# Kernel tuning notes

Measured on AMD Instinct MI355X. Metric: run time of the kernel, lower is better.

The kernel has to match this reference:

```python
import jax, jax.numpy as jnp
import numpy as np

N = 50000       # nodes
E = 800000      # edges
D = 128         # in_channels == hidden*heads
H = 8           # heads
C = 16          # hidden_channels (per-head dim)
L = 4           # num_layers
OUT = 128       # out_channels


def setup_inputs() -> dict:
    key = jax.random.key(0)
    ks = jax.random.split(key, 16)
    s = 1.0 / np.sqrt(D)
    inp = {
        "x": jax.random.normal(ks[0], (N, D), dtype=jnp.float32),
        "edge_index": jax.random.randint(ks[1], (2, E), 0, N, dtype=jnp.int32),
        "batch": jnp.zeros((N,), dtype=jnp.int32),
        # stacked per-layer params (all layers are D->H*C with D == H*C)
        "Wq": jax.random.normal(ks[2], (L, D, H * C), dtype=jnp.float32) * s,
        "bq": jnp.zeros((L, H * C), dtype=jnp.float32),
        "Wk": jax.random.normal(ks[3], (L, D, H * C), dtype=jnp.float32) * s,
        "bk": jnp.zeros((L, H * C), dtype=jnp.float32),
        "Wv": jax.random.normal(ks[4], (L, D, H * C), dtype=jnp.float32) * s,
        "bv": jnp.zeros((L, H * C), dtype=jnp.float32),
        "Wskip": jax.random.normal(ks[5], (L, D, H * C), dtype=jnp.float32) * s,
        "bskip": jnp.zeros((L, H * C), dtype=jnp.float32),
        "Wout": jax.random.normal(ks[6], (D, OUT), dtype=jnp.float32) * s,
        "bout": jnp.zeros((OUT,), dtype=jnp.float32),
    }
    return inp


def _transformer_conv(x, src, dst, Wq, bq, Wk, bk, Wv, bv, Wskip, bskip):
    # PyG TransformerConv (concat=True, root_weight=True, beta=False), eval mode
    q = (x @ Wq + bq).reshape(N, H, C)
    k = (x @ Wk + bk).reshape(N, H, C)
    v = (x @ Wv + bv).reshape(N, H, C)
    # edge-wise attention scores [E, H]
    score = jnp.einsum("ehc,ehc->eh", q[dst], k[src]) / jnp.sqrt(jnp.float32(C))
    # segment softmax over incoming edges of each dst node
    m = jax.ops.segment_max(score, dst, num_segments=N)          # [N, H]
    p = jnp.exp(score - m[dst])                                  # [E, H]
    z = jax.ops.segment_sum(p, dst, num_segments=N)              # [N, H]
    alpha = p / z[dst]                                           # [E, H]
    msg = alpha[:, :, None] * v[src]                             # [E, H, C]
    agg = jax.ops.segment_sum(msg, dst, num_segments=N)          # [N, H, C]
    return agg.reshape(N, H * C) + (x @ Wskip + bskip)


def reference(x, edge_index, batch, Wq, bq, Wk, bk, Wv, bv, Wskip, bskip, Wout, bout):
    src = edge_index[0]
    dst = edge_index[1]
    for l in range(L):
        x = _transformer_conv(x, src, dst, Wq[l], bq[l], Wk[l], bk[l],
                              Wv[l], bv[l], Wskip[l], bskip[l])
        x = jax.nn.relu(x)  # dropout is identity in eval mode
    return x @ Wout + bout
```

## Files before the change

kernel.cpp:

```cpp
#include <hip/hip_runtime.h>
#include <hip/hip_fp16.h>
#include <math.h>

#define NN 50000
#define EE 800000
#define DD 128

typedef __attribute__((ext_vector_type(8))) _Float16 half8;
typedef __attribute__((ext_vector_type(2))) _Float16 h2;
typedef __attribute__((ext_vector_type(4))) float f32x4;

#if __has_builtin(__builtin_amdgcn_fdot2)
#define FDOT2(a,b,c) __builtin_amdgcn_fdot2((a),(b),(c),false)
#else
static __device__ __forceinline__ float FDOT2(h2 a, h2 b, float c){
  return c + (float)a[0]*(float)b[0] + (float)a[1]*(float)b[1];
}
#endif


__global__ void zero_kernel(int* __restrict__ p, int n){
  int i = blockIdx.x*blockDim.x + threadIdx.x;
  if (i < n) p[i] = 0;
}

__global__ void hist_kernel(const int* __restrict__ edst, int* __restrict__ deg, int e){
  int i = blockIdx.x*blockDim.x + threadIdx.x;
  if (i < e) atomicAdd(&deg[edst[i]], 1);
}

__global__ void scan_partial(const int* __restrict__ deg, int* __restrict__ bsum, int n){
  __shared__ int s[256];
  int t = threadIdx.x;
  int i = blockIdx.x*256 + t;
  s[t] = (i < n) ? deg[i] : 0;
  __syncthreads();
  for (int o = 128; o > 0; o >>= 1){
    if (t < o) s[t] += s[t+o];
    __syncthreads();
  }
  if (t == 0) bsum[blockIdx.x] = s[0];
}

__global__ void scan_bsums(int* __restrict__ bsum, int nb){
  __shared__ int s[256];
  int t = threadIdx.x;
  int v = (t < nb) ? bsum[t] : 0;
  s[t] = v;
  __syncthreads();
  for (int o = 1; o < 256; o <<= 1){
    int x = (t >= o) ? s[t-o] : 0;
    __syncthreads();
    s[t] += x;
    __syncthreads();
  }
  if (t < nb) bsum[t] = s[t] - v;
}

__global__ void scan_apply(const int* __restrict__ deg, const int* __restrict__ bsum,
                           int* __restrict__ off, int* __restrict__ cursor, int n){
  __shared__ int s[256];
  int t = threadIdx.x;
  int i = blockIdx.x*256 + t;
  int v = (i < n) ? deg[i] : 0;
  s[t] = v;
  __syncthreads();
  for (int o = 1; o < 256; o <<= 1){
    int x = (t >= o) ? s[t-o] : 0;
    __syncthreads();
    s[t] += x;
    __syncthreads();
  }
  int excl = s[t] - v + bsum[blockIdx.x];
  if (i < n){
    off[i] = excl;
    if (i < n-1) cursor[i] = excl;
  }
}

__global__ void scatter_kernel(const int* __restrict__ esrc, const int* __restrict__ edst,
                               int* __restrict__ cursor, int* __restrict__ csr_src, int e){
  int i = blockIdx.x*blockDim.x + threadIdx.x;
  if (i < e){
    int d = edst[i];
    int pos = atomicAdd(&cursor[d], 1);
    csr_src[pos] = esrc[i];
  }
}

__global__ void prep_w(const float* __restrict__ Wq, const float* __restrict__ Wk,
                       const float* __restrict__ Wv, const float* __restrict__ Ws,
                       const float* __restrict__ bq, const float* __restrict__ bk,
                       const float* __restrict__ bv, const float* __restrict__ bs,
                       const float* __restrict__ Wout,
                       __half* __restrict__ wt, float* __restrict__ bcat,
                       __half* __restrict__ wtout){
  int idx = blockIdx.x*256 + threadIdx.x;
  if (idx < 4*512*128){
    int l = idx >> 16;
    int rem = idx & 65535;
    int n = rem >> 7;
    int k = rem & 127;
    int mat = n >> 7;
    int nn = n & 127;
    const float* W = (mat==0)?Wq:(mat==1)?Wk:(mat==2)?Wv:Ws;
    wt[idx] = __float2half(W[l*16384 + k*128 + nn]);
  }
  if (idx < 128*128){
    int n = idx >> 7, k = idx & 127;
    wtout[idx] = __float2half(Wout[k*128 + n]);
  }
  if (idx < 4*512){
    int l = idx >> 9, n = idx & 511;
    int mat = n >> 7, nn = n & 127;
    const float* B = (mat==0)?bq:(mat==1)?bk:(mat==2)?bv:bs;
    bcat[idx] = B[l*128 + nn];
  }
}

__global__ void convert_x(const float* __restrict__ x, __half* __restrict__ xh, int n8){
  int i = blockIdx.x*256 + threadIdx.x;
  if (i < n8){
    float4 f0 = *(const float4*)&x[(size_t)i*8];
    float4 f1 = *(const float4*)&x[(size_t)i*8+4];
    __half2 h[4] = {__floats2half2_rn(f0.x,f0.y), __floats2half2_rn(f0.z,f0.w),
                    __floats2half2_rn(f1.x,f1.y), __floats2half2_rn(f1.z,f1.w)};
    *(int4*)&xh[(size_t)i*8] = *(const int4*)h;
  }
}

template<int FMODE>
__global__ __launch_bounds__(256) void mfma_gemm(
    const __half* __restrict__ xh, const __half* __restrict__ wt,
    const float* __restrict__ bias,
    __half* __restrict__ oq, __half* __restrict__ okv, __half* __restrict__ osk,
    float* __restrict__ ofp, int nrows)
{
  __shared__ __half a_lds[64*128];
  __shared__ __half b_lds[128*128];

  const int tid = threadIdx.x;
  const int m0 = blockIdx.x * 64;
  const int lane = tid & 63;
  const int w  = tid >> 6;
  const int wr = w >> 1, wc = w & 1;
  const int li = lane & 15, lg = lane >> 4;

  #pragma unroll
  for (int p = 0; p < 4; p++){
    int chunk = tid + p*256;
    int row = chunk >> 4;
    int cs  = chunk & 15;
    int gm = m0 + row;
    int4 va = make_int4(0,0,0,0);
    if (gm < nrows) va = *(const int4*)&xh[(size_t)gm*DD + cs*8];
    *(int4*)&a_lds[row*128 + (cs ^ (row & 7))*8] = va;
  }

  const int NMATS = (FMODE == 0) ? 4 : 1;
  for (int mat = 0; mat < NMATS; mat++){
    #pragma unroll
    for (int p = 0; p < 8; p++){
      int chunk = tid + p*256;
      int row = chunk >> 4;
      int cs  = chunk & 15;
      int4 vb = *(const int4*)&wt[(size_t)(mat*128 + row)*DD + cs*8];
      *(int4*)&b_lds[row*128 + (cs ^ (row & 7))*8] = vb;
    }
    __syncthreads();

    f32x4 acc[2][4];
    #pragma unroll
    for (int fn = 0; fn < 4; fn++){
      float b = bias[mat*128 + wc*64 + fn*16 + li];
      #pragma unroll
      for (int fm = 0; fm < 2; fm++)
        acc[fm][fn] = (f32x4){b, b, b, b};
    }

    #pragma unroll
    for (int kk = 0; kk < 4; kk++){
      half8 af[2], bf[4];
      #pragma unroll
      for (int fm = 0; fm < 2; fm++){
        int row = wr*32 + fm*16 + li;
        int chunk = kk*4 + lg;
        af[fm] = *(half8*)&a_lds[row*128 + (chunk ^ (row & 7))*8];
      }
      #pragma unroll
      for (int fn = 0; fn < 4; fn++){
        int row = wc*64 + fn*16 + li;
        int chunk = kk*4 + lg;
        bf[fn] = *(half8*)&b_lds[row*128 + (chunk ^ (row & 7))*8];
      }
      #pragma unroll
      for (int fm = 0; fm < 2; fm++)
        #pragma unroll
        for (int fn = 0; fn < 4; fn++)
          acc[fm][fn] = __builtin_amdgcn_mfma_f32_16x16x32_f16(af[fm], bf[fn], acc[fm][fn], 0, 0, 0);
    }
    __syncthreads();

    if (FMODE == 0){
      #pragma unroll
      for (int fm = 0; fm < 2; fm++)
        #pragma unroll
        for (int fn = 0; fn < 4; fn++)
          #pragma unroll
          for (int r = 0; r < 4; r++){
            int row = wr*32 + fm*16 + lg*4 + r;
            int col = wc*64 + fn*16 + li;
            int chunk = col >> 3, within = col & 7;
            b_lds[row*128 + (chunk ^ (row & 7))*8 + within] = __float2half(acc[fm][fn][r]);
          }
      __syncthreads();
      #pragma unroll
      for (int p = 0; p < 4; p++){
        int chunk = tid + p*256;
        int row = chunk >> 4, cs = chunk & 15;
        int gm = m0 + row;
        if (gm < nrows){
          int4 val = *(int4*)&b_lds[row*128 + (cs ^ (row & 7))*8];
          if (mat == 0)      *(int4*)&oq [(size_t)gm*128 + cs*8]       = val;
          else if (mat == 1) *(int4*)&okv[(size_t)gm*256 + cs*8]       = val;
          else if (mat == 2) *(int4*)&okv[(size_t)gm*256 + 128 + cs*8] = val;
          else               *(int4*)&osk[(size_t)gm*128 + cs*8]       = val;
        }
      }
      __syncthreads();
    } else {
      float* f_lds = (float*)b_lds;
      #pragma unroll
      for (int fm = 0; fm < 2; fm++)
        #pragma unroll
        for (int fn = 0; fn < 4; fn++)
          #pragma unroll
          for (int r = 0; r < 4; r++){
            int row = wr*32 + fm*16 + lg*4 + r;
            int col = wc*64 + fn*16 + li;
            int chunk = col >> 2, within = col & 3;
            f_lds[row*128 + (chunk ^ (row & 7))*4 + within] = acc[fm][fn][r];
          }
      __syncthreads();
      #pragma unroll
      for (int p = 0; p < 8; p++){
        int chunk = tid + p*256;
        int row = chunk >> 5, cs = chunk & 31;
        int gm = m0 + row;
        if (gm < nrows)
          *(int4*)&ofp[(size_t)gm*DD + cs*4] = *(int4*)&f_lds[row*128 + (cs ^ (row & 7))*4];
      }
    }
  }
}

__global__ __launch_bounds__(256) void agg_kernel(
    const __half* __restrict__ hq, const __half* __restrict__ hsk,
    const __half* __restrict__ kv,
    const int* __restrict__ off, const int* __restrict__ csr_src,
    __half* __restrict__ xout, int n)
{
  int wid = blockIdx.x*4 + (threadIdx.x >> 6);
  if (wid >= n) return;
  int lane = threadIdx.x & 63;
  int sub  = lane >> 3;
  int h    = lane & 7;
  int c    = h*16;

  int4 q0 = *(const int4*)&hq[(size_t)wid*DD + c];
  int4 q1 = *(const int4*)&hq[(size_t)wid*DD + c + 8];
  const h2* qh0 = (const h2*)&q0;
  const h2* qh1 = (const h2*)&q1;

  float z = 0.f;
  float acc[16];
  #pragma unroll
  for (int i = 0; i < 16; i++) acc[i] = 0.f;

  const int e1 = off[wid+1];
  int e = off[wid] + sub;
  int s2 = (e+8 < e1) ? csr_src[e+8] : -1;
  int4 k0r, k1r, v0r, v1r;
  if (e < e1){
    const __half* r = kv + (size_t)csr_src[e]*256 + c;
    k0r = *(const int4*)r;        k1r = *(const int4*)(r+8);
    v0r = *(const int4*)(r+128);  v1r = *(const int4*)(r+136);
  }
  while (e < e1){
    int4 k0n, k1n, v0n, v1n;
    if (s2 >= 0){
      const __half* r = kv + (size_t)s2*256 + c;
      k0n = *(const int4*)r;        k1n = *(const int4*)(r+8);
      v0n = *(const int4*)(r+128);  v1n = *(const int4*)(r+136);
    }
    int s3 = (e+16 < e1) ? csr_src[e+16] : -1;

    const h2* kh0 = (const h2*)&k0r;
    const h2* kh1 = (const h2*)&k1r;
    float p = 0.f;
    #pragma unroll
    for (int i = 0; i < 4; i++) p = FDOT2(kh0[i], qh0[i], p);
    #pragma unroll
    for (int i = 0; i < 4; i++) p = FDOT2(kh1[i], qh1[i], p);
    float wgt = __expf(p * 0.25f);

    const __half2* vh0 = (const __half2*)&v0r;
    const __half2* vh1 = (const __half2*)&v1r;
    #pragma unroll
    for (int i = 0; i < 4; i++){
      float2 f = __half22float2(vh0[i]);
      acc[2*i]   += wgt * f.x;
      acc[2*i+1] += wgt * f.y;
    }
    #pragma unroll
    for (int i = 0; i < 4; i++){
      float2 f = __half22float2(vh1[i]);
      acc[8+2*i]   += wgt * f.x;
      acc[8+2*i+1] += wgt * f.y;
    }
    z += wgt;

    k0r = k0n; k1r = k1n; v0r = v0n; v1r = v1n;
    s2 = s3; e += 8;
  }

  #pragma unroll
  for (int d = 8; d <= 32; d <<= 1){
    z += __shfl_xor(z, d);
    #pragma unroll
    for (int i = 0; i < 16; i++)
      acc[i] += __shfl_xor(acc[i], d);
  }

  if (sub == 0){
    float inv = (z > 0.f) ? 1.f/z : 0.f;
    int4 s0 = *(const int4*)&hsk[(size_t)wid*DD + c];
    int4 s1 = *(const int4*)&hsk[(size_t)wid*DD + c + 8];
    const __half2* sh0 = (const __half2*)&s0;
    const __half2* sh1 = (const __half2*)&s1;
    __half2 po[4];
    #pragma unroll
    for (int i = 0; i < 4; i++){
      float2 s = __half22float2(sh0[i]);
      po[i] = __floats2half2_rn(fmaxf(acc[2*i]*inv + s.x, 0.f),
                                fmaxf(acc[2*i+1]*inv + s.y, 0.f));
    }
    *(int4*)&xout[(size_t)wid*DD + c] = *(const int4*)po;
    #pragma unroll
    for (int i = 0; i < 4; i++){
      float2 s = __half22float2(sh1[i]);
      po[i] = __floats2half2_rn(fmaxf(acc[8+2*i]*inv + s.x, 0.f),
                                fmaxf(acc[8+2*i+1]*inv + s.y, 0.f));
    }
    *(int4*)&xout[(size_t)wid*DD + c + 8] = *(const int4*)po;
  }
}


extern "C" void kernel_launch(void* const* d_in, const int* in_sizes, int n_in,
                              void* d_out, int out_size, void* d_ws, size_t ws_size,
                              hipStream_t stream) {
  const float* x     = (const float*)d_in[0];
  const int*   edge  = (const int*)d_in[1];
  const int*   esrc  = edge;
  const int*   edst  = edge + EE;
  const float* Wq    = (const float*)d_in[3];
  const float* bq    = (const float*)d_in[4];
  const float* Wk    = (const float*)d_in[5];
  const float* bk    = (const float*)d_in[6];
  const float* Wv    = (const float*)d_in[7];
  const float* bv    = (const float*)d_in[8];
  const float* Wsk   = (const float*)d_in[9];
  const float* bsk   = (const float*)d_in[10];
  const float* Wout  = (const float*)d_in[11];
  const float* bout  = (const float*)d_in[12];
  float* out = (float*)d_out;

  uintptr_t base = (uintptr_t)d_ws;
  auto align = [](uintptr_t p){ return (p + 255) & ~(uintptr_t)255; };
  int* deg    = (int*)base;  base = align(base + (NN+1)*sizeof(int));
  int* off    = (int*)base;  base = align(base + (NN+1)*sizeof(int));
  int* cursor = (int*)base;  base = align(base + NN*sizeof(int));
  int* bsum   = (int*)base;  base = align(base + 256*sizeof(int));
  int* csr    = (int*)base;  base = align(base + (size_t)EE*sizeof(int));
  __half* xh   = (__half*)base; base = align(base + (size_t)NN*DD*sizeof(__half));
  __half* xbuf = (__half*)base; base = align(base + (size_t)NN*DD*sizeof(__half));
  __half* hq   = (__half*)base; base = align(base + (size_t)NN*DD*sizeof(__half));
  __half* hsk  = (__half*)base; base = align(base + (size_t)NN*DD*sizeof(__half));
  __half* kvb  = (__half*)base; base = align(base + (size_t)NN*256*sizeof(__half));
  __half* wt   = (__half*)base; base = align(base + (size_t)4*512*128*sizeof(__half));
  __half* wtout= (__half*)base; base = align(base + (size_t)128*128*sizeof(__half));
  float*  bcat = (float*)base;  base = align(base + (size_t)4*512*sizeof(float));

  const int NP = NN + 1;
  const int SCAN_BLKS = (NP + 255)/256;

  zero_kernel<<<SCAN_BLKS, 256, 0, stream>>>(deg, NP);
  hist_kernel<<<(EE+255)/256, 256, 0, stream>>>(edst, deg, EE);
  scan_partial<<<SCAN_BLKS, 256, 0, stream>>>(deg, bsum, NP);
  scan_bsums<<<1, 256, 0, stream>>>(bsum, SCAN_BLKS);
  scan_apply<<<SCAN_BLKS, 256, 0, stream>>>(deg, bsum, off, cursor, NP);
  scatter_kernel<<<(EE+255)/256, 256, 0, stream>>>(esrc, edst, cursor, csr, EE);

  prep_w<<<1024, 256, 0, stream>>>(Wq, Wk, Wv, Wsk, bq, bk, bv, bsk, Wout, wt, bcat, wtout);
  convert_x<<<(NN*DD/8 + 255)/256, 256, 0, stream>>>(x, xh, NN*DD/8);

  const int MT64 = (NN + 63)/64;
  const __half* xin = xh;
  for (int l = 0; l < 4; l++){
    mfma_gemm<0><<<MT64, 256, 0, stream>>>(
        xin, wt + (size_t)l*512*128, bcat + l*512,
        hq, kvb, hsk, nullptr, NN);
    agg_kernel<<<(NN+3)/4, 256, 0, stream>>>(hq, hsk, kvb, off, csr, xbuf, NN);
    xin = xbuf;
  }
  mfma_gemm<1><<<MT64, 256, 0, stream>>>(
      xin, wtout, bout, nullptr, nullptr, nullptr, out, NN);
}
```

Baseline: 437.3 us.

## Store K/V head-major and split aggregation per head across blocks

The GEMM epilogue now writes K and V in a head-major layout ([head][node][k16|v16]), so each head's key and value sit together in one contiguous 64-byte chunk per source node. The aggregation kernel launches one block per (head, 4-node group): each wavefront processes 16 edges at once with 4 lanes per edge, and blockIdx.x&7 spreads consecutive blocks across heads. The aim is a smaller per-head working set for the random gathers, which may improve L2 hit rates, plus more parallelism per node. In exchange, csr offsets and indices are read 8 times (once per head), the q loads are redundant, and the old software prefetch of the next edge's K/V is dropped.

```diff
diff --git a/kernel.cpp b/kernel.cpp
--- a/kernel.cpp
+++ b/kernel.cpp
@@ -221,10 +221,13 @@
         int gm = m0 + row;
         if (gm < nrows){
           int4 val = *(int4*)&b_lds[row*128 + (cs ^ (row & 7))*8];
-          if (mat == 0)      *(int4*)&oq [(size_t)gm*128 + cs*8]       = val;
-          else if (mat == 1) *(int4*)&okv[(size_t)gm*256 + cs*8]       = val;
-          else if (mat == 2) *(int4*)&okv[(size_t)gm*256 + 128 + cs*8] = val;
-          else               *(int4*)&osk[(size_t)gm*128 + cs*8]       = val;
+          if (mat == 0)      *(int4*)&oq [(size_t)gm*128 + cs*8] = val;
+          else if (mat == 3) *(int4*)&osk[(size_t)gm*128 + cs*8] = val;
+          else {
+            int h = cs >> 1, half = cs & 1;
+            size_t base = ((size_t)h*NN + gm)*32 + ((mat==2) ? 16 : 0);
+            *(int4*)&okv[base + half*8] = val;
+          }
         }
       }
       __syncthreads();
@@ -256,103 +259,72 @@
 
 __global__ __launch_bounds__(256) void agg_kernel(
     const __half* __restrict__ hq, const __half* __restrict__ hsk,
-    const __half* __restrict__ kv,
+    const __half* __restrict__ kvh,
     const int* __restrict__ off, const int* __restrict__ csr_src,
     __half* __restrict__ xout, int n)
 {
-  int wid = blockIdx.x*4 + (threadIdx.x >> 6);
-  if (wid >= n) return;
-  int lane = threadIdx.x & 63;
-  int sub  = lane >> 3;
-  int h    = lane & 7;
-  int c    = h*16;
-
-  int4 q0 = *(const int4*)&hq[(size_t)wid*DD + c];
-  int4 q1 = *(const int4*)&hq[(size_t)wid*DD + c + 8];
-  const h2* qh0 = (const h2*)&q0;
-  const h2* qh1 = (const h2*)&q1;
+  const int h  = blockIdx.x & 7;
+  const int nd = (blockIdx.x >> 3)*4 + (threadIdx.x >> 6);
+  if (nd >= n) return;
+  const int lane  = threadIdx.x & 63;
+  const int eslot = lane >> 2;
+  const int part  = lane & 3;
+
+  int4 qr = make_int4(0,0,0,0);
+  if (part < 2) qr = *(const int4*)&hq[(size_t)nd*DD + h*16 + part*8];
+  const h2* qq = (const h2*)&qr;
 
   float z = 0.f;
-  float acc[16];
+  float acc[8] = {0.f,0.f,0.f,0.f,0.f,0.f,0.f,0.f};
+
+  const int e0 = off[nd], e1 = off[nd+1];
+  const __half* kvbase = kvh + (size_t)h*NN*32;
+  for (int eb = e0; eb < e1; eb += 16){
+    int e = eb + eslot;
+    bool valid = e < e1;
+    int ee = valid ? e : (e1 - 1);
+    int s = csr_src[ee];
+    int4 d = *(const int4*)&kvbase[(size_t)s*32 + part*8];
+
+    const h2* kd = (const h2*)&d;
+    float p = 0.f;
+    #pragma unroll
+    for (int i = 0; i < 4; i++) p = FDOT2(kd[i], qq[i], p);
+    p += __shfl_xor(p, 1);
+    float wgt = valid ? __expf(p * 0.25f) : 0.f;
+    float wv  = __shfl_xor(wgt, 2);
+
+    const __half2* vd = (const __half2*)&d;
+    #pragma unroll
+    for (int i = 0; i < 4; i++){
+      float2 f = __half22float2(vd[i]);
+      acc[2*i]   += wv * f.x;
+      acc[2*i+1] += wv * f.y;
+    }
+    z += wv;
+  }
+
   #pragma unroll
-  for (int i = 0; i < 16; i++) acc[i] = 0.f;
-
-  const int e1 = off[wid+1];
-  int e = off[wid] + sub;
-  int s2 = (e+8 < e1) ? csr_src[e+8] : -1;
-  int4 k0r, k1r, v0r, v1r;
-  if (e < e1){
-    const __half* r = kv + (size_t)csr_src[e]*256 + c;
-    k0r = *(const int4*)r;        k1r = *(const int4*)(r+8);
-    v0r = *(const int4*)(r+128);  v1r = *(const int4*)(r+136);
-  }
-  while (e < e1){
-    int4 k0n, k1n, v0n, v1n;
-    if (s2 >= 0){
-      const __half* r = kv + (size_t)s2*256 + c;
-      k0n = *(const int4*)r;        k1n = *(const int4*)(r+8);
-      v0n = *(const int4*)(r+128);  v1n = *(const int4*)(r+136);
-    }
-    int s3 = (e+16 < e1) ? csr_src[e+16] : -1;
-
-    const h2* kh0 = (const h2*)&k0r;
-    const h2* kh1 = (const h2*)&k1r;
-    float p = 0.f;
-    #pragma unroll
-    for (int i = 0; i < 4; i++) p = FDOT2(kh0[i], qh0[i], p);
-    #pragma unroll
-    for (int i = 0; i < 4; i++) p = FDOT2(kh1[i], qh1[i], p);
-    float wgt = __expf(p * 0.25f);
-
-    const __half2* vh0 = (const __half2*)&v0r;
-    const __half2* vh1 = (const __half2*)&v1r;
+  for (int d = 4; d <= 32; d <<= 1){
+    z += __shfl_xor(z, d);
+    #pragma unroll
+    for (int i = 0; i < 8; i++)
+      acc[i] += __shfl_xor(acc[i], d);
+  }
+
+  if (eslot == 0 && part >= 2){
+    float inv = (z > 0.f) ? 1.f/z : 0.f;
+    int co = h*16 + (part-2)*8;
+    int4 sr = *(const int4*)&hsk[(size_t)nd*DD + co];
+    const __half2* sh2 = (const __half2*)&sr;
+    __half2 po[4];
     #pragma unroll
     for (int i = 0; i < 4; i++){
-      float2 f = __half22float2(vh0[i]);
-      acc[2*i]   += wgt * f.x;
-      acc[2*i+1] += wgt * f.y;
-    }
-    #pragma unroll
-    for (int i = 0; i < 4; i++){
-      float2 f = __half22float2(vh1[i]);
-      acc[8+2*i]   += wgt * f.x;
-      acc[8+2*i+1] += wgt * f.y;
-    }
-    z += wgt;
-
-    k0r = k0n; k1r = k1n; v0r = v0n; v1r = v1n;
-    s2 = s3; e += 8;
-  }
-
-  #pragma unroll
-  for (int d = 8; d <= 32; d <<= 1){
-    z += __shfl_xor(z, d);
-    #pragma unroll
-    for (int i = 0; i < 16; i++)
-      acc[i] += __shfl_xor(acc[i], d);
-  }
-
-  if (sub == 0){
-    float inv = (z > 0.f) ? 1.f/z : 0.f;
-    int4 s0 = *(const int4*)&hsk[(size_t)wid*DD + c];
-    int4 s1 = *(const int4*)&hsk[(size_t)wid*DD + c + 8];
-    const __half2* sh0 = (const __half2*)&s0;
-    const __half2* sh1 = (const __half2*)&s1;
-    __half2 po[4];
-    #pragma unroll
-    for (int i = 0; i < 4; i++){
-      float2 s = __half22float2(sh0[i]);
+      float2 s = __half22float2(sh2[i]);
       po[i] = __floats2half2_rn(fmaxf(acc[2*i]*inv + s.x, 0.f),
                                 fmaxf(acc[2*i+1]*inv + s.y, 0.f));
     }
-    *(int4*)&xout[(size_t)wid*DD + c] = *(const int4*)po;
-    #pragma unroll
-    for (int i = 0; i < 4; i++){
-      float2 s = __half22float2(sh1[i]);
-      po[i] = __floats2half2_rn(fmaxf(acc[8+2*i]*inv + s.x, 0.f),
-                                fmaxf(acc[8+2*i+1]*inv + s.y, 0.f));
-    }
-    *(int4*)&xout[(size_t)wid*DD + c + 8] = *(const int4*)po;
+    *(int4*)&xout[(size_t)nd*DD + co] = *(const int4*)po;
   }
 }
 
@@ -387,7 +359,7 @@
   __half* xbuf = (__half*)base; base = align(base + (size_t)NN*DD*sizeof(__half));
   __half* hq   = (__half*)base; base = align(base + (size_t)NN*DD*sizeof(__half));
   __half* hsk  = (__half*)base; base = align(base + (size_t)NN*DD*sizeof(__half));
-  __half* kvb  = (__half*)base; base = align(base + (size_t)NN*256*sizeof(__half));
+  __half* kvh  = (__half*)base; base = align(base + (size_t)NN*256*sizeof(__half));
   __half* wt   = (__half*)base; base = align(base + (size_t)4*512*128*sizeof(__half));
   __half* wtout= (__half*)base; base = align(base + (size_t)128*128*sizeof(__half));
   float*  bcat = (float*)base;  base = align(base + (size_t)4*512*sizeof(float));
@@ -406,12 +378,13 @@
   convert_x<<<(NN*DD/8 + 255)/256, 256, 0, stream>>>(x, xh, NN*DD/8);
 
   const int MT64 = (NN + 63)/64;
+  const int AGG_BLKS = ((NN + 3)/4) * 8;
   const __half* xin = xh;
   for (int l = 0; l < 4; l++){
     mfma_gemm<0><<<MT64, 256, 0, stream>>>(
         xin, wt + (size_t)l*512*128, bcat + l*512,
-        hq, kvb, hsk, nullptr, NN);
-    agg_kernel<<<(NN+3)/4, 256, 0, stream>>>(hq, hsk, kvb, off, csr, xbuf, NN);
+        hq, kvh, hsk, nullptr, NN);
+    agg_kernel<<<AGG_BLKS, 256, 0, stream>>>(hq, hsk, kvh, off, csr, xbuf, NN);
     xin = xbuf;
   }
   mfma_gemm<1><<<MT64, 256, 0, stream>>>(
```

Measured after the change: 879.5 us. +101.1%, slower.
